# Kernel optimization log

Hardware: AMD Instinct MI355X
Metric: run time of the kernel (lower is better)

The kernel has to match this reference:

```python
import jax, jax.numpy as jnp
import numpy as np
from jax import lax

B, C, D, NH, H, W = 32, 768, 512, 4, 24, 24
HD = C // NH          # 192
FHW = H * W           # 576 (must equal 24*24 per o_proj_img2)


def _p(key, shape, scale=0.02):
    return scale * jax.random.normal(key, shape, dtype=jnp.float32)


def setup_inputs() -> dict:
    ks = jax.random.split(jax.random.key(0), 10)
    return dict(
        img_feats=jax.random.normal(ks[0], (B, C, H, W), jnp.float32),
        txt_feats=jax.random.normal(ks[1], (B, D), jnp.float32),
        fn_w=jnp.ones((C,), jnp.float32), fn_b=jnp.zeros((C,), jnp.float32),
        gn_w=jnp.ones((D,), jnp.float32), gn_b=jnp.zeros((D,), jnp.float32),
        qkv_img_w=_p(ks[2], (3 * C, C)),
        qkv_txt_w=_p(ks[3], (3 * C, D)),
        o_img_w=_p(ks[4], (C, C)), o_img_b=jnp.zeros((C,), jnp.float32),
        o_img2_w=_p(ks[5], (FHW, HD)), o_img2_b=jnp.zeros((FHW,), jnp.float32),
        ffn_norm_w=jnp.ones((C,), jnp.float32), ffn_norm_b=jnp.zeros((C,), jnp.float32),
        fc1_w=_p(ks[6], (C, C)),
        dw_w=_p(ks[7], (C, 1, 3, 3)),
        fc2_w=_p(ks[8], (C, C)),
    )


def layernorm2d(x, w, b, eps=1e-6):
    # normalize over channel dim (dim 1) of NCHW
    u = x.mean(1, keepdims=True)
    s = ((x - u) ** 2).mean(1, keepdims=True)
    x = (x - u) * lax.rsqrt(s + eps)
    return w[:, None, None] * x + b[:, None, None]


def l2norm_last(x, eps=1e-12):
    # F.normalize(x, dim=-1): divide by L2 norm clamped at eps
    n = jnp.sqrt(jnp.sum(x * x, axis=-1, keepdims=True))
    return x / jnp.maximum(n, eps)


def _forward(img_feats, txt_feats, fn_w, fn_b, gn_w, gn_b, qkv_img_w, qkv_txt_w,
             o_img_w, o_img_b, o_img2_w, o_img2_b, ffn_norm_w, ffn_norm_b,
             fc1_w, dw_w, fc2_w):
    x = layernorm2d(img_feats, fn_w, fn_b)
    # guide LayerNorm (torch default eps=1e-5, biased var)
    mu = txt_feats.mean(-1, keepdims=True)
    var = jnp.mean((txt_feats - mu) ** 2, axis=-1, keepdims=True)
    t = (txt_feats - mu) * lax.rsqrt(var + 1e-5) * gn_w + gn_b

    # qkv img: 1x1 conv; channel layout (ng nh hd) -> [B,3,NH,HD,F]
    qkv_img = jnp.einsum('bchw,oc->bohw', x, qkv_img_w).reshape(B, 3, NH, HD, FHW)
    q_img, k_img, v_img = qkv_img[:, 0], qkv_img[:, 1], qkv_img[:, 2]

    # qkv txt: layout 'b (nh (ng hd))' per the two rearranges -> [B,NH,3,HD]
    qkv_txt = (t @ qkv_txt_w.T).reshape(B, NH, 3, HD)
    q_txt, k_txt = qkv_txt[:, :, 0], qkv_txt[:, :, 1]

    # normalize over size-1 trailing dim == x / max(|x|, eps)  (sign-like)
    nq_txt = q_txt / jnp.maximum(jnp.abs(q_txt), 1e-12)          # [B,NH,HD]
    nk_img = l2norm_last(k_img)                                  # [B,NH,HD,F]
    # einsum('bnhd,bnhf->bnhf') with d of size 1 == broadcast multiply over h
    attn1 = jax.nn.softmax(nq_txt[..., None] * nk_img, axis=-1)  # [B,NH,HD,F]
    txt_on_img = jnp.einsum('bnhf,bngf->bnhg', attn1, v_img)     # [B,NH,HD,HD]

    nk_txt = k_txt / jnp.maximum(jnp.abs(k_txt), 1e-12)
    nq_img = l2norm_last(q_img)
    attn2 = jax.nn.softmax(nk_txt[..., None] * nq_img, axis=-1)
    txt_to_img2 = jnp.einsum('bnhf,bngf->bnhg', attn2, v_img)

    img = (txt_on_img + txt_to_img2).reshape(B, NH * HD, HD)     # [B,768,192]
    y = (img @ o_img2_w.T + o_img2_b).reshape(B, C, H, W)        # [B,768,24,24]
    out = jnp.einsum('bchw,oc->bohw', y, o_img_w) + o_img_b[None, :, None, None] + img_feats

    # ConvMlp FFN (mlp_times=1, bias=False convs, exact GELU)
    z = layernorm2d(out, ffn_norm_w, ffn_norm_b)
    z = jnp.einsum('bchw,oc->bohw', z, fc1_w)
    z = lax.conv_general_dilated(z, dw_w, (1, 1), 'SAME',
                                 feature_group_count=C,
                                 dimension_numbers=('NCHW', 'OIHW', 'NCHW'))
    z = jax.nn.gelu(z, approximate=False)
    z = jnp.einsum('bchw,oc->bohw', z, fc2_w)
    return out + z


def reference(img_feats, txt_feats, fn_w, fn_b, gn_w, gn_b, qkv_img_w, qkv_txt_w,
              o_img_w, o_img_b, o_img2_w, o_img2_b, ffn_norm_w, ffn_norm_b,
              fc1_w, dw_w, fc2_w):
    return _forward(img_feats, txt_feats, fn_w, fn_b, gn_w, gn_b, qkv_img_w,
                    qkv_txt_w, o_img_w, o_img_b, o_img2_w, o_img2_b,
                    ffn_norm_w, ffn_norm_b, fc1_w, dw_w, fc2_w)
```

## Files before the change

kernel.cpp:

```cpp
#include <hip/hip_runtime.h>

typedef unsigned short u16;
typedef __attribute__((ext_vector_type(8))) short short8_t;
typedef __attribute__((ext_vector_type(4))) float f32x4;
typedef __attribute__((ext_vector_type(4))) unsigned short u16x4;

static constexpr int cB   = 32;
static constexpr int cC   = 768;
static constexpr int cD   = 512;
static constexpr int cNH  = 4;
static constexpr int cHD  = 192;
static constexpr int cFHW = 576;
static constexpr int cC3  = 2304;

__device__ inline float us2f(u16 s) {
    union { unsigned int u; float f; } v; v.u = ((unsigned int)s) << 16; return v.f;
}
__device__ inline u16 f2bf(float f) {
    union { float f; unsigned int u; } v; v.f = f;
    unsigned int r = v.u + 0x7FFFu + ((v.u >> 16) & 1u);
    return (u16)(r >> 16);
}
__device__ inline float ldflex(const void* p, size_t i, int isf32) {
    return isf32 ? ((const float*)p)[i] : us2f(((const u16*)p)[i]);
}

__device__ inline void gload16(const void* g, void* l) {
    __builtin_amdgcn_global_load_lds(
        (const __attribute__((address_space(1))) void*)g,
        (__attribute__((address_space(3))) void*)l, 16, 0, 0);
}

__global__ void detect_kernel(const u16* __restrict__ raw, int* __restrict__ flags) {
    flags[0] = (raw[0] == 0x3F80u) ? 0 : 1;
}

struct FlatDesc { const void* src[12]; float* dst[12]; int off[13]; };
__global__ __launch_bounds__(256) void flatten_kernel(FlatDesc d, const int* __restrict__ flags) {
    const int isf = flags[0];
    const int gid = blockIdx.x * 256 + threadIdx.x;
    if (gid >= d.off[12]) return;
    int s = 0;
    #pragma unroll
    for (int i = 1; i < 12; i++) s += (gid >= d.off[i]) ? 1 : 0;
    const int j = gid - d.off[s];
    d.dst[s][j] = ldflex(d.src[s], j, isf);
}

__global__ __launch_bounds__(256) void cast_bf16_kernel(
    const void* __restrict__ src, u16* __restrict__ dst, int n, const int* __restrict__ flags)
{
    const int isf = flags[0];
    for (int i = blockIdx.x * 256 + threadIdx.x; i < n; i += gridDim.x * 256)
        dst[i] = isf ? f2bf(((const float*)src)[i]) : ((const u16*)src)[i];
}

__global__ __launch_bounds__(256) void fold_cast_kernel(
    const void* __restrict__ src, const float* __restrict__ gamma,
    u16* __restrict__ dst, int n, const int* __restrict__ flags)
{
    const int isf = flags[0];
    for (int i = blockIdx.x * 256 + threadIdx.x; i < n; i += gridDim.x * 256) {
        const int c = i % cC;
        dst[i] = f2bf(ldflex(src, i, isf) * gamma[c]);
    }
}

__global__ __launch_bounds__(64) void bias_fold_kernel(
    const void* __restrict__ W, const float* __restrict__ gamma, const float* __restrict__ beta,
    float* __restrict__ B1, float* __restrict__ B2, const int* __restrict__ flags)
{
    const int m = blockIdx.x, lane = threadIdx.x, isf = flags[0];
    float s1 = 0.f, s2 = 0.f;
    for (int c = lane; c < cC; c += 64) {
        const float wv = ldflex(W, (size_t)m * cC + c, isf);
        s1 += wv * beta[c]; s2 += wv * gamma[c];
    }
    #pragma unroll
    for (int o = 1; o < 64; o <<= 1) { s1 += __shfl_xor(s1, o, 64); s2 += __shfl_xor(s2, o, 64); }
    if (lane == 0) { B1[m] = s1; B2[m] = s2; }
}

__global__ __launch_bounds__(256) void transpose_kernel(
    const void* __restrict__ src, float* __restrict__ dst,
    int Mdim, int Kdim, const int* __restrict__ flags)
{
    __shared__ float t[32][33];
    const int isf = flags[0];
    const int k0 = blockIdx.x * 32, m0 = blockIdx.y * 32;
    const int x = threadIdx.x & 31, y = threadIdx.x >> 5;
    #pragma unroll
    for (int i = 0; i < 4; i++) {
        const int m = y + i * 8;
        t[m][x] = ldflex(src, (size_t)(m0 + m) * Kdim + k0 + x, isf);
    }
    __syncthreads();
    #pragma unroll
    for (int i = 0; i < 4; i++) {
        const int r = y + i * 8;
        dst[(size_t)(k0 + r) * Mdim + m0 + x] = t[x][r];
    }
}

__global__ __launch_bounds__(256) void txt_ln_kernel(
    const float* __restrict__ txt, const float* __restrict__ gw, const float* __restrict__ gb,
    float* __restrict__ tln)
{
    __shared__ float red[8];
    const int b = blockIdx.x, tid = threadIdx.x;
    const float v0 = txt[(size_t)b * cD + tid];
    const float v1 = txt[(size_t)b * cD + 256 + tid];
    float s = v0 + v1, ss = v0 * v0 + v1 * v1;
    #pragma unroll
    for (int o = 1; o < 64; o <<= 1) { s += __shfl_xor(s, o, 64); ss += __shfl_xor(ss, o, 64); }
    const int wid = tid >> 6, lane = tid & 63;
    if (lane == 0) { red[wid] = s; red[4 + wid] = ss; }
    __syncthreads();
    s  = red[0] + red[1] + red[2] + red[3];
    ss = red[4] + red[5] + red[6] + red[7];
    const float mean = s * (1.f / cD);
    const float var  = fmaxf(ss * (1.f / cD) - mean * mean, 0.f);
    const float r = rsqrtf(var + 1e-5f);
    tln[(size_t)b * cD + tid]       = (v0 - mean) * r * gw[tid]       + gb[tid];
    tln[(size_t)b * cD + 256 + tid] = (v1 - mean) * r * gw[tid + 256] + gb[tid + 256];
}

__global__ __launch_bounds__(256) void txt_gemm_kernel(
    const float* __restrict__ Wt, const float* __restrict__ tln, float* __restrict__ out)
{
    const int o  = blockIdx.x * 256 + threadIdx.x;
    const int b0 = blockIdx.y * 8;
    __shared__ float t[8][cD];
    for (int i = threadIdx.x; i < 8 * cD; i += 256)
        t[i >> 9][i & (cD - 1)] = tln[(size_t)(b0 + (i >> 9)) * cD + (i & (cD - 1))];
    __syncthreads();
    float acc[8] = {};
    #pragma unroll 2
    for (int k = 0; k < cD; k += 4) {
        const float w0 = Wt[(size_t)(k + 0) * cC3 + o];
        const float w1 = Wt[(size_t)(k + 1) * cC3 + o];
        const float w2 = Wt[(size_t)(k + 2) * cC3 + o];
        const float w3 = Wt[(size_t)(k + 3) * cC3 + o];
        #pragma unroll
        for (int b = 0; b < 8; b++) {
            const float4 tv = *(const float4*)&t[b][k];
            acc[b] += w0 * tv.x + w1 * tv.y + w2 * tv.z + w3 * tv.w;
        }
    }
    #pragma unroll
    for (int b = 0; b < 8; b++) out[(size_t)(b0 + b) * cC3 + o] = acc[b];
}

__global__ __launch_bounds__(1024) void ln_stats_kernel(
    const void* __restrict__ x, size_t xoff, float* __restrict__ mr,
    const int* __restrict__ flags)
{
    const int isf = flags[0];
    const int b = blockIdx.y;
    const int l = threadIdx.x & 63;
    const int f = (blockIdx.x << 6) + l;
    const int cg = threadIdx.x >> 6;
    const size_t base = xoff + (size_t)b * cC * cFHW + f;
    float s = 0.f, ss = 0.f;
    for (int c = cg; c < cC; c += 16) {
        float v = ldflex(x, base + (size_t)c * cFHW, isf);
        s += v; ss += v * v;
    }
    __shared__ float S[16][64], SS[16][64];
    S[cg][l] = s; SS[cg][l] = ss;
    __syncthreads();
    if (threadIdx.x < 64) {
        float su = 0.f, sq = 0.f;
        #pragma unroll
        for (int i = 0; i < 16; i++) { su += S[i][l]; sq += SS[i][l]; }
        const float mean = su * (1.f / cC);
        const float var  = fmaxf(sq * (1.f / cC) - mean * mean, 0.f);
        float* o = mr + ((size_t)b * cFHW + f) * 2;
        o[0] = mean; o[1] = rsqrtf(var + 1e-6f);
    }
}

__global__ __launch_bounds__(256) void ln_stats_rows_kernel(
    const u16* __restrict__ Xt, float* __restrict__ mr)
{
    const int wid = threadIdx.x >> 6, lane = threadIdx.x & 63;
    const size_t row = (size_t)blockIdx.x * 4 + wid;
    const u16* r = Xt + row * cC;
    float s = 0.f, ss = 0.f;
    const short8_t a = *(const short8_t*)(r + lane * 8);
    const u16x4 bq   = *(const u16x4*)(r + 512 + lane * 4);
    #pragma unroll
    for (int j = 0; j < 8; j++) { const float v = us2f((u16)a[j]); s += v; ss += v * v; }
    #pragma unroll
    for (int j = 0; j < 4; j++) { const float v = us2f(bq[j]); s += v; ss += v * v; }
    #pragma unroll
    for (int o = 1; o < 64; o <<= 1) { s += __shfl_xor(s, o, 64); ss += __shfl_xor(ss, o, 64); }
    if (lane == 0) {
        const float mean = s * (1.f / cC);
        const float var  = fmaxf(ss * (1.f / cC) - mean * mean, 0.f);
        mr[row * 2] = mean; mr[row * 2 + 1] = rsqrtf(var + 1e-6f);
    }
}

template <int XSRC>
__global__ __launch_bounds__(256) void prep_xt_kernel(
    const void* __restrict__ X, size_t xoff, u16* __restrict__ Xt,
    const float* __restrict__ mr, const float* __restrict__ lnw, const float* __restrict__ lnb,
    const int* __restrict__ flags)
{
    __shared__ float t[64][33];
    const int isf = (XSRC == 2) ? flags[0] : 1;
    const int f0 = blockIdx.x * 32, c0 = blockIdx.y * 64, b = blockIdx.z;
    const int tid = threadIdx.x;
    const int fx = tid & 31, cy = tid >> 5;
    const size_t base = (size_t)b * cC * cFHW;
    #pragma unroll
    for (int i = 0; i < 8; i++) {
        const int c = c0 + cy + i * 8;
        const size_t ei = base + (size_t)c * cFHW + f0 + fx;
        t[cy + i * 8][fx] = (XSRC == 2) ? ldflex(X, xoff + ei, isf) : ((const float*)X)[ei];
    }
    __syncthreads();
    const int cx = tid & 31, fy = tid >> 5;
    #pragma unroll
    for (int i = 0; i < 4; i++) {
        const int fl = fy + i * 8;
        const int f = f0 + fl;
        float v0 = t[cx * 2][fl], v1 = t[cx * 2 + 1][fl];
        if (XSRC == 2) {
            const float* mp = mr + ((size_t)b * cFHW + f) * 2;
            const float mean = mp[0], rst = mp[1];
            v0 = (v0 - mean) * rst * lnw[c0 + cx * 2]     + lnb[c0 + cx * 2];
            v1 = (v1 - mean) * rst * lnw[c0 + cx * 2 + 1] + lnb[c0 + cx * 2 + 1];
        }
        const unsigned int pk = (unsigned int)f2bf(v0) | ((unsigned int)f2bf(v1) << 16);
        *(unsigned int*)(Xt + base + (size_t)f * cC + c0 + cx * 2) = pk;
    }
}

template <int EPI>
__global__ __launch_bounds__(256, 2) void conv_mfma(
    const u16* __restrict__ Wb, const u16* __restrict__ Xt,
    float* __restrict__ outp, const float* __restrict__ bias_m,
    const void* __restrict__ resRaw, size_t resOff, const float* __restrict__ resF,
    u16* __restrict__ vout,
    const float* __restrict__ aff_mr, const float* __restrict__ aff_B1, const float* __restrict__ aff_B2,
    int M, int K, int Mt, const int* __restrict__ flags)
{
    const int nwg = 9 * Mt;
    int wg = blockIdx.x;
    {
        const int q = nwg >> 3, r = nwg & 7, x = wg & 7, idx = wg >> 3;
        wg = (x < r ? x * (q + 1) : r * (q + 1) + (x - r) * q) + idx;
    }
    const int xt = wg / Mt, yt = wg - xt * Mt;
    const int n0 = xt * 64, m0 = yt * 256, b = blockIdx.z;

    __shared__ __align__(16) u16 A_s[2][256 * 64];
    __shared__ __align__(16) u16 B_s[2][64 * 64];

    const int tid = threadIdx.x;
    const int w = tid >> 6, lane = tid & 63, lq = lane >> 4, lr = lane & 15;
    const int l8 = lane >> 3, c8 = lane & 7;
    const int xch = ((c8 ^ l8) << 4);

    const u16* wbase = Wb + (size_t)m0 * K;
    const u16* xbase = Xt + ((size_t)b * cFHW + n0) * K;

    f32x4 acc[4][4];
    #pragma unroll
    for (int i = 0; i < 4; i++)
        #pragma unroll
        for (int j = 0; j < 4; j++)
            acc[i][j] = (f32x4)0.f;

    const int nt = K >> 6;

    #pragma unroll
    for (int j = 0; j < 8; ++j) {
        const int r = w * 64 + j * 8 + l8;
        gload16((const char*)(wbase + (size_t)r * K) + xch, (char*)&A_s[0][(w * 64 + j * 8) * 64]);
    }
    #pragma unroll
    for (int j = 0; j < 2; ++j) {
        const int r = w * 16 + j * 8 + l8;
        gload16((const char*)(xbase + (size_t)r * K) + xch, (char*)&B_s[0][(w * 16 + j * 8) * 64]);
    }

    int buf = 0;
    #pragma unroll 1
    for (int t = 0; t < nt; ++t) {
        if (t + 1 < nt) {
            const int k0 = (t + 1) << 6;
            #pragma unroll
            for (int j = 0; j < 8; ++j) {
                const int r = w * 64 + j * 8 + l8;
                gload16((const char*)(wbase + (size_t)r * K + k0) + xch,
                        (char*)&A_s[buf ^ 1][(w * 64 + j * 8) * 64]);
            }
            #pragma unroll
            for (int j = 0; j < 2; ++j) {
                const int r = w * 16 + j * 8 + l8;
                gload16((const char*)(xbase + (size_t)r * K + k0) + xch,
                        (char*)&B_s[buf ^ 1][(w * 16 + j * 8) * 64]);
            }
            asm volatile("s_waitcnt vmcnt(10)" ::: "memory");
        } else {
            asm volatile("s_waitcnt vmcnt(0)" ::: "memory");
        }
        __builtin_amdgcn_s_barrier();
        __builtin_amdgcn_sched_barrier(0);
        __builtin_amdgcn_s_setprio(1);
        const u16* As = &A_s[buf][0];
        const u16* Bs = &B_s[buf][0];
        #pragma unroll
        for (int kk = 0; kk < 2; kk++) {
            short8_t af[4], bfr[4];
            #pragma unroll
            for (int fm = 0; fm < 4; fm++) {
                const int ml = w * 64 + fm * 16 + lr;
                af[fm] = *(const short8_t*)((const char*)As + ml * 128 + ((kk * 64 + lq * 16) ^ ((lr & 7) << 4)));
            }
            #pragma unroll
            for (int fn = 0; fn < 4; fn++) {
                const int nl = fn * 16 + lr;
                bfr[fn] = *(const short8_t*)((const char*)Bs + nl * 128 + ((kk * 64 + lq * 16) ^ ((lr & 7) << 4)));
            }
            #pragma unroll
            for (int fm = 0; fm < 4; fm++)
                #pragma unroll
                for (int fn = 0; fn < 4; fn++)
                    acc[fm][fn] = __builtin_amdgcn_mfma_f32_16x16x32_bf16(af[fm], bfr[fn], acc[fm][fn], 0, 0, 0);
        }
        __builtin_amdgcn_s_setprio(0);
        __builtin_amdgcn_s_barrier();
        buf ^= 1;
    }

    const int mrow0 = m0 + w * 64;

    if constexpr (EPI == 5) {
        #pragma unroll
        for (int fm = 0; fm < 4; fm++)
            #pragma unroll
            for (int fn = 0; fn < 4; fn++)
                #pragma unroll
                for (int i = 0; i < 4; i++) {
                    const int mg = mrow0 + fm * 16 + lq * 4 + i;
                    vout[((size_t)b * M + mg) * cFHW + n0 + fn * 16 + lr] = f2bf(acc[fm][fn][i]);
                }
        return;
    }
    if constexpr (EPI == 4) {
        float b1r[4][4], b2r[4][4];
        #pragma unroll
        for (int fm = 0; fm < 4; fm++)
            #pragma unroll
            for (int i = 0; i < 4; i++) {
                const int mg = mrow0 + fm * 16 + lq * 4 + i;
                b1r[fm][i] = aff_B1[mg];
                b2r[fm][i] = aff_B2[mg];
            }
        #pragma unroll
        for (int fn = 0; fn < 4; fn++) {
            const int nn = n0 + fn * 16 + lr;
            const float2 ms = *(const float2*)(aff_mr + ((size_t)b * cFHW + nn) * 2);
            const float sf = ms.y, mean_sf = ms.x * ms.y;
            #pragma unroll
            for (int fm = 0; fm < 4; fm++)
                #pragma unroll
                for (int i = 0; i < 4; i++) {
                    const int mg = mrow0 + fm * 16 + lq * 4 + i;
                    outp[((size_t)b * M + mg) * cFHW + nn] =
                        sf * acc[fm][fn][i] + b1r[fm][i] - mean_sf * b2r[fm][i];
                }
        }
        return;
    }
    if constexpr (EPI == 1) {
        const int isf = flags[0];
        #pragma unroll
        for (int fm = 0; fm < 4; fm++) {
            #pragma unroll
            for (int fn = 0; fn < 4; fn++) {
                const int nn = n0 + fn * 16 + lr;
                u16x4 pk;
                #pragma unroll
                for (int i = 0; i < 4; i++) {
                    const int mg = mrow0 + fm * 16 + lq * 4 + i;
                    const size_t o = ((size_t)b * M + mg) * cFHW + nn;
                    const float vv = acc[fm][fn][i] + bias_m[mg] + ldflex(resRaw, resOff + o, isf);
                    outp[o] = vv;
                    pk[i] = f2bf(vv);
                }
                *(u16x4*)(vout + ((size_t)b * cFHW + nn) * cC + (mrow0 + fm * 16 + lq * 4)) = pk;
            }
        }
        return;
    }
    #pragma unroll
    for (int fm = 0; fm < 4; fm++) {
        #pragma unroll
        for (int fn = 0; fn < 4; fn++) {
            #pragma unroll
            for (int i = 0; i < 4; i++) {
                const int mg = mrow0 + fm * 16 + lq * 4 + i;
                const size_t o = ((size_t)b * M + mg) * cFHW + n0 + fn * 16 + lr;
                float vv = acc[fm][fn][i];
                if constexpr (EPI == 2) vv += resF[o];
                outp[o] = vv;
            }
        }
    }
}

__global__ __launch_bounds__(64) void attn_p_kernel(
    const u16* __restrict__ qkv, const float* __restrict__ tq, u16* __restrict__ Pbf)
{
    const int idx = blockIdx.x;
    const int h = idx % cHD;
    const int bn = idx / cHD;
    const int n = bn & 3, b = bn >> 2;
    const int lane = threadIdx.x;
    const u16* qrow = qkv + ((size_t)b * cC3 + n * cHD + h) * cFHW;
    const u16* krow = qkv + ((size_t)b * cC3 + cC + n * cHD + h) * cFHW;
    float kvr[9], qvr[9];
    #pragma unroll
    for (int j = 0; j < 9; j++) {
        kvr[j] = us2f(krow[lane + j * 64]);
        qvr[j] = us2f(qrow[lane + j * 64]);
    }
    float ssk = 0.f, mink = 3.0e38f, maxk = -3.0e38f;
    float ssq = 0.f, minq = 3.0e38f, maxq = -3.0e38f;
    #pragma unroll
    for (int j = 0; j < 9; j++) {
        const float kv = kvr[j]; ssk += kv * kv; maxk = fmaxf(maxk, kv); mink = fminf(mink, kv);
        const float qv = qvr[j]; ssq += qv * qv; maxq = fmaxf(maxq, qv); minq = fminf(minq, qv);
    }
    #pragma unroll
    for (int o = 1; o < 64; o <<= 1) {
        ssk += __shfl_xor(ssk, o, 64); ssq += __shfl_xor(ssq, o, 64);
        maxk = fmaxf(maxk, __shfl_xor(maxk, o, 64)); mink = fminf(mink, __shfl_xor(mink, o, 64));
        maxq = fmaxf(maxq, __shfl_xor(maxq, o, 64)); minq = fminf(minq, __shfl_xor(minq, o, 64));
    }
    const float qt = tq[(size_t)b * cC3 + n * 3 * cHD + h];
    const float kt = tq[(size_t)b * cC3 + n * 3 * cHD + cHD + h];
    const float sign1 = qt / fmaxf(fabsf(qt), 1e-12f);
    const float sign2 = kt / fmaxf(fabsf(kt), 1e-12f);
    const float a1 = sign1 / fmaxf(sqrtf(ssk), 1e-12f);
    const float a2 = sign2 / fmaxf(sqrtf(ssq), 1e-12f);
    const float m1 = fmaxf(a1 * maxk, a1 * mink);
    const float m2 = fmaxf(a2 * maxq, a2 * minq);
    float e1[9], e2[9];
    float z1 = 0.f, z2 = 0.f;
    #pragma unroll
    for (int j = 0; j < 9; j++) {
        e1[j] = expf(a1 * kvr[j] - m1); z1 += e1[j];
        e2[j] = expf(a2 * qvr[j] - m2); z2 += e2[j];
    }
    #pragma unroll
    for (int o = 1; o < 64; o <<= 1) { z1 += __shfl_xor(z1, o, 64); z2 += __shfl_xor(z2, o, 64); }
    const float iz1 = 1.f / z1, iz2 = 1.f / z2;
    u16* prow = Pbf + ((size_t)b * cC + n * cHD + h) * cFHW;
    #pragma unroll
    for (int j = 0; j < 9; j++)
        prow[lane + j * 64] = f2bf(e1[j] * iz1 + e2[j] * iz2);
}

__global__ __launch_bounds__(256, 2) void pv_mfma(
    const u16* __restrict__ P, const u16* __restrict__ qkv, u16* __restrict__ img, int nbn)
{
    const int nwg = 3 * nbn;
    int wg = blockIdx.x;
    {
        const int q = nwg >> 3, r = nwg & 7, x = wg & 7, idx = wg >> 3;
        wg = (x < r ? x * (q + 1) : r * (q + 1) + (x - r) * q) + idx;
    }
    const int bn = wg / 3, gt = wg - bn * 3;
    const int g0 = gt * 64;
    const int b = bn >> 2, n = bn & 3;

    __shared__ __align__(16) u16 A_s[2][192 * 64];
    __shared__ __align__(16) u16 B_s[2][64 * 64];

    const int tid = threadIdx.x;
    const int w = tid >> 6, lane = tid & 63, lq = lane >> 4, lr = lane & 15;
    const int l8 = lane >> 3, c8 = lane & 7;
    const int xch = ((c8 ^ l8) << 4);

    const u16* pbase = P + ((size_t)b * cC + n * cHD) * cFHW;
    const u16* vbase = qkv + ((size_t)b * cC3 + 2 * cC + n * cHD + g0) * cFHW;

    f32x4 acc[3][4];
    #pragma unroll
    for (int i = 0; i < 3; i++)
        #pragma unroll
        for (int j = 0; j < 4; j++)
            acc[i][j] = (f32x4)0.f;

    const int nt = cFHW / 64;

    #pragma unroll
    for (int j = 0; j < 6; ++j) {
        const int r = w * 48 + j * 8 + l8;
        gload16((const char*)(pbase + (size_t)r * cFHW) + xch, (char*)&A_s[0][(w * 48 + j * 8) * 64]);
    }
    #pragma unroll
    for (int j = 0; j < 2; ++j) {
        const int r = w * 16 + j * 8 + l8;
        gload16((const char*)(vbase + (size_t)r * cFHW) + xch, (char*)&B_s[0][(w * 16 + j * 8) * 64]);
    }

    int buf = 0;
    #pragma unroll 1
    for (int t = 0; t < nt; ++t) {
        if (t + 1 < nt) {
            const int k0 = (t + 1) << 6;
            #pragma unroll
            for (int j = 0; j < 6; ++j) {
                const int r = w * 48 + j * 8 + l8;
                gload16((const char*)(pbase + (size_t)r * cFHW + k0) + xch,
                        (char*)&A_s[buf ^ 1][(w * 48 + j * 8) * 64]);
            }
            #pragma unroll
            for (int j = 0; j < 2; ++j) {
                const int r = w * 16 + j * 8 + l8;
                gload16((const char*)(vbase + (size_t)r * cFHW + k0) + xch,
                        (char*)&B_s[buf ^ 1][(w * 16 + j * 8) * 64]);
            }
            asm volatile("s_waitcnt vmcnt(8)" ::: "memory");
        } else {
            asm volatile("s_waitcnt vmcnt(0)" ::: "memory");
        }
        __builtin_amdgcn_s_barrier();
        __builtin_amdgcn_sched_barrier(0);
        __builtin_amdgcn_s_setprio(1);
        const u16* As = &A_s[buf][0];
        const u16* Bs = &B_s[buf][0];
        #pragma unroll
        for (int kk = 0; kk < 2; kk++) {
            short8_t af[3], bfr[4];
            #pragma unroll
            for (int fm = 0; fm < 3; fm++) {
                const int ml = w * 48 + fm * 16 + lr;
                af[fm] = *(const short8_t*)((const char*)As + ml * 128 + ((kk * 64 + lq * 16) ^ ((lr & 7) << 4)));
            }
            #pragma unroll
            for (int fn = 0; fn < 4; fn++) {
                const int nl = fn * 16 + lr;
                bfr[fn] = *(const short8_t*)((const char*)Bs + nl * 128 + ((kk * 64 + lq * 16) ^ ((lr & 7) << 4)));
            }
            #pragma unroll
            for (int fm = 0; fm < 3; fm++)
                #pragma unroll
                for (int fn = 0; fn < 4; fn++)
                    acc[fm][fn] = __builtin_amdgcn_mfma_f32_16x16x32_bf16(af[fm], bfr[fn], acc[fm][fn], 0, 0, 0);
        }
        __builtin_amdgcn_s_setprio(0);
        __builtin_amdgcn_s_barrier();
        buf ^= 1;
    }

    #pragma unroll
    for (int fm = 0; fm < 3; fm++)
        #pragma unroll
        for (int fn = 0; fn < 4; fn++)
            #pragma unroll
            for (int i = 0; i < 4; i++) {
                const int mm = w * 48 + fm * 16 + lq * 4 + i;
                img[((size_t)b * cC + n * cHD + mm) * cHD + g0 + fn * 16 + lr] = f2bf(acc[fm][fn][i]);
            }
}

__global__ __launch_bounds__(256, 2) void y_mfma(
    const u16* __restrict__ img, const u16* __restrict__ o2w,
    const float* __restrict__ bias_n, u16* __restrict__ Xt)
{
    const int nwg = 9 * 3;
    int wg = blockIdx.x;
    {
        const int q = nwg >> 3, r = nwg & 7, x = wg & 7, idx = wg >> 3;
        wg = (x < r ? x * (q + 1) : r * (q + 1) + (x - r) * q) + idx;
    }
    const int xt = wg / 3, yt = wg - xt * 3;
    const int n0 = xt * 64, m0 = yt * 256, b = blockIdx.z;
    constexpr int K = cHD;

    __shared__ __align__(16) u16 A_s[2][256 * 64];
    __shared__ __align__(16) u16 B_s[2][64 * 64];

    const int tid = threadIdx.x;
    const int w = tid >> 6, lane = tid & 63, lq = lane >> 4, lr = lane & 15;
    const int l8 = lane >> 3, c8 = lane & 7;
    const int xch = ((c8 ^ l8) << 4);

    const u16* abase = img + ((size_t)b * cC + m0) * K;
    const u16* bbase = o2w + (size_t)n0 * K;

    f32x4 acc[4][4];
    #pragma unroll
    for (int i = 0; i < 4; i++)
        #pragma unroll
        for (int j = 0; j < 4; j++)
            acc[i][j] = (f32x4)0.f;

    const int nt = K >> 6;

    #pragma unroll
    for (int j = 0; j < 8; ++j) {
        const int r = w * 64 + j * 8 + l8;
        gload16((const char*)(abase + (size_t)r * K) + xch, (char*)&A_s[0][(w * 64 + j * 8) * 64]);
    }
    #pragma unroll
    for (int j = 0; j < 2; ++j) {
        const int r = w * 16 + j * 8 + l8;
        gload16((const char*)(bbase + (size_t)r * K) + xch, (char*)&B_s[0][(w * 16 + j * 8) * 64]);
    }

    int buf = 0;
    #pragma unroll 1
    for (int t = 0; t < nt; ++t) {
        if (t + 1 < nt) {
            const int k0 = (t + 1) << 6;
            #pragma unroll
            for (int j = 0; j < 8; ++j) {
                const int r = w * 64 + j * 8 + l8;
                gload16((const char*)(abase + (size_t)r * K + k0) + xch,
                        (char*)&A_s[buf ^ 1][(w * 64 + j * 8) * 64]);
            }
            #pragma unroll
            for (int j = 0; j < 2; ++j) {
                const int r = w * 16 + j * 8 + l8;
                gload16((const char*)(bbase + (size_t)r * K + k0) + xch,
                        (char*)&B_s[buf ^ 1][(w * 16 + j * 8) * 64]);
            }
            asm volatile("s_waitcnt vmcnt(10)" ::: "memory");
        } else {
            asm volatile("s_waitcnt vmcnt(0)" ::: "memory");
        }
        __builtin_amdgcn_s_barrier();
        __builtin_amdgcn_sched_barrier(0);
        __builtin_amdgcn_s_setprio(1);
        const u16* As = &A_s[buf][0];
        const u16* Bs = &B_s[buf][0];
        #pragma unroll
        for (int kk = 0; kk < 2; kk++) {
            short8_t af[4], bfr[4];
            #pragma unroll
            for (int fm = 0; fm < 4; fm++) {
                const int ml = w * 64 + fm * 16 + lr;
                af[fm] = *(const short8_t*)((const char*)As + ml * 128 + ((kk * 64 + lq * 16) ^ ((lr & 7) << 4)));
            }
            #pragma unroll
            for (int fn = 0; fn < 4; fn++) {
                const int nl = fn * 16 + lr;
                bfr[fn] = *(const short8_t*)((const char*)Bs + nl * 128 + ((kk * 64 + lq * 16) ^ ((lr & 7) << 4)));
            }
            #pragma unroll
            for (int fm = 0; fm < 4; fm++)
                #pragma unroll
                for (int fn = 0; fn < 4; fn++)
                    acc[fm][fn] = __builtin_amdgcn_mfma_f32_16x16x32_bf16(af[fm], bfr[fn], acc[fm][fn], 0, 0, 0);
        }
        __builtin_amdgcn_s_setprio(0);
        __builtin_amdgcn_s_barrier();
        buf ^= 1;
    }

    #pragma unroll
    for (int fm = 0; fm < 4; fm++) {
        #pragma unroll
        for (int fn = 0; fn < 4; fn++) {
            const int nn = n0 + fn * 16 + lr;
            const float bn_ = bias_n[nn];
            u16x4 pk;
            #pragma unroll
            for (int i = 0; i < 4; i++) pk[i] = f2bf(acc[fm][fn][i] + bn_);
            const int mm = m0 + w * 64 + fm * 16 + lq * 4;
            *(u16x4*)(Xt + ((size_t)b * cFHW + nn) * cC + mm) = pk;
        }
    }
}

__global__ __launch_bounds__(576) void dwconv_gelu_kernel(
    const float* __restrict__ X, const float* __restrict__ w, float* __restrict__ Y)
{
    const int c = blockIdx.x, b = blockIdx.y;
    __shared__ float t[26][28];
    const int tid = threadIdx.x;
    float* tf = &t[0][0];
    for (int i = tid; i < 26 * 28; i += 576) tf[i] = 0.f;
    __syncthreads();
    const size_t base = ((size_t)b * cC + c) * cFHW;
    const int x = tid % 24, y = tid / 24;
    t[y + 1][x + 1] = X[base + tid];
    __syncthreads();
    float w9[9];
    #pragma unroll
    for (int j = 0; j < 9; j++) w9[j] = w[c * 9 + j];
    float s = 0.f;
    #pragma unroll
    for (int dy = 0; dy < 3; dy++)
        #pragma unroll
        for (int dx = 0; dx < 3; dx++)
            s += w9[dy * 3 + dx] * t[y + dy][x + dx];
    const float g = 0.5f * s * (1.f + erff(s * 0.70710678118654752f));
    Y[base + tid] = g;
}

extern "C" void kernel_launch(void* const* d_in, const int* in_sizes, int n_in,
                              void* d_out, int out_size, void* d_ws, size_t ws_size,
                              hipStream_t stream)
{
    char* p = (char*)d_ws;
    auto allocB = [&](size_t bytes) { char* r = p; p += (bytes + 255) & ~(size_t)255; return r; };
    float* c_txt   = (float*)allocB((size_t)cB * cD * 4);
    float* c_fnw   = (float*)allocB(cC * 4);
    float* c_fnb   = (float*)allocB(cC * 4);
    float* c_gnw   = (float*)allocB(cD * 4);
    float* c_gnb   = (float*)allocB(cD * 4);
    float* c_oib   = (float*)allocB(cC * 4);
    float* c_oi2w  = (float*)allocB((size_t)cFHW * cHD * 4);
    float* c_oi2b  = (float*)allocB(cFHW * 4);
    float* c_ffnw  = (float*)allocB(cC * 4);
    float* c_ffnb  = (float*)allocB(cC * 4);
    float* c_dw    = (float*)allocB(cC * 9 * 4);
    u16*   w_qkv_bf = (u16*)allocB((size_t)cC3 * cC * 2);
    u16*   w_oi_bf  = (u16*)allocB((size_t)cC * cC * 2);
    u16*   w_fc1_bf = (u16*)allocB((size_t)cC * cC * 2);
    u16*   w_fc2_bf = (u16*)allocB((size_t)cC * cC * 2);
    u16*   w_o2w_bf = (u16*)allocB((size_t)cFHW * cHD * 2);
    float* t_qkvtw = (float*)allocB((size_t)cD * cC3 * 4);
    float* tln     = (float*)allocB((size_t)cB * cD * 4);
    int*   flags   = (int*)allocB(256);
    float* tq      = (float*)allocB((size_t)cB * cC3 * 4);
    float* mr1     = (float*)allocB((size_t)cB * cFHW * 2 * 4);
    float* mr2     = (float*)allocB((size_t)cB * cFHW * 2 * 4);
    float* b1f     = (float*)allocB(cC * 4);
    float* b2f     = (float*)allocB(cC * 4);
    const size_t fixedBytes = (size_t)(p - (char*)d_ws);
    auto needBytes = [&](int Q) {
        return fixedBytes
             + (size_t)Q * (cC3 + cC) * cFHW * 2ull
             + (size_t)Q * cC * cFHW * 4ull * 2ull
             + (size_t)Q * cC * cHD * 2ull
             + (size_t)Q * cC * cFHW * 2ull
             + 8192;
    };
    int Q = 8;
    if (ws_size >= needBytes(32)) Q = 32;
    else if (ws_size >= needBytes(16)) Q = 16;
    const size_t QCF = (size_t)Q * cC * cFHW;
    char*  qkvreg = allocB((size_t)Q * (cC3 + cC) * cFHW * 2);
    u16*   qkvbf = (u16*)qkvreg;
    u16*   Pbf   = (u16*)(qkvreg + (size_t)Q * cC3 * cFHW * 2);
    float* A2    = (float*)qkvreg;
    float* A0    = (float*)allocB(QCF * 4);
    float* A1    = (float*)allocB(QCF * 4);
    u16*   imgbf = (u16*)allocB((size_t)Q * cC * cHD * 2);
    u16*   XtA   = (u16*)allocB(QCF * 2);
    (void)in_sizes; (void)n_in; (void)out_size;

    detect_kernel<<<1, 1, 0, stream>>>((const u16*)d_in[2], flags);

    FlatDesc fd;
    const void* srcs[11] = { d_in[1], d_in[2], d_in[3], d_in[4], d_in[5],
                             d_in[9], d_in[10], d_in[11], d_in[12], d_in[13], d_in[15] };
    float* dsts[11]      = { c_txt, c_fnw, c_fnb, c_gnw, c_gnb,
                             c_oib, c_oi2w, c_oi2b, c_ffnw, c_ffnb, c_dw };
    const int ns[11]     = { cB * cD, cC, cC, cD, cD,
                             cC, cFHW * cHD, cFHW, cC, cC, cC * 9 };
    int tot = 0;
    for (int i = 0; i < 11; i++) { fd.src[i] = srcs[i]; fd.dst[i] = dsts[i]; fd.off[i] = tot; tot += ns[i]; }
    fd.src[11] = srcs[0]; fd.dst[11] = dsts[0];
    fd.off[11] = tot; fd.off[12] = tot;
    flatten_kernel<<<(tot + 255) / 256, 256, 0, stream>>>(fd, flags);

    cast_bf16_kernel<<<512, 256, 0, stream>>>(d_in[6],  w_qkv_bf, cC3 * cC, flags);
    cast_bf16_kernel<<<256, 256, 0, stream>>>(d_in[8],  w_oi_bf,  cC * cC, flags);
    fold_cast_kernel<<<256, 256, 0, stream>>>(d_in[14], c_ffnw, w_fc1_bf, cC * cC, flags);
    cast_bf16_kernel<<<256, 256, 0, stream>>>(d_in[16], w_fc2_bf, cC * cC, flags);
    cast_bf16_kernel<<<128, 256, 0, stream>>>(d_in[10], w_o2w_bf, cFHW * cHD, flags);
    bias_fold_kernel<<<cC, 64, 0, stream>>>(d_in[14], c_ffnw, c_ffnb, b1f, b2f, flags);

    transpose_kernel<<<dim3(cD / 32, cC3 / 32), 256, 0, stream>>>(d_in[7], t_qkvtw, cC3, cD, flags);
    txt_ln_kernel<<<cB, 256, 0, stream>>>(c_txt, c_gnw, c_gnb, tln);
    txt_gemm_kernel<<<dim3(cC3 / 256, cB / 8), 256, 0, stream>>>(t_qkvtw, tln, tq);

    for (int q0 = 0; q0 < cB; q0 += Q) {
        const size_t off = (size_t)q0 * cC * cFHW;
        u16* XtB = (u16*)((float*)d_out + off);
        ln_stats_kernel<<<dim3(9, Q), 1024, 0, stream>>>(d_in[0], off, mr1, flags);
        prep_xt_kernel<2><<<dim3(cFHW / 32, cC / 64, Q), 256, 0, stream>>>(
            d_in[0], off, XtA, mr1, c_fnw, c_fnb, flags);
        conv_mfma<5><<<dim3(9 * (cC3 / 256), 1, Q), 256, 0, stream>>>(
            w_qkv_bf, XtA, nullptr, nullptr, nullptr, 0, nullptr, qkvbf,
            nullptr, nullptr, nullptr, cC3, cC, cC3 / 256, flags);
        attn_p_kernel<<<Q * cNH * cHD, 64, 0, stream>>>(qkvbf, tq + (size_t)q0 * cC3, Pbf);
        pv_mfma<<<3 * Q * cNH, 256, 0, stream>>>(Pbf, qkvbf, imgbf, Q * cNH);
        y_mfma<<<dim3(27, 1, Q), 256, 0, stream>>>(imgbf, w_o2w_bf, c_oi2b, XtA);
        conv_mfma<1><<<dim3(9 * (cC / 256), 1, Q), 256, 0, stream>>>(
            w_oi_bf, XtA, A0, c_oib, d_in[0], off, nullptr, XtB,
            nullptr, nullptr, nullptr, cC, cC, cC / 256, flags);
        ln_stats_rows_kernel<<<Q * cFHW / 4, 256, 0, stream>>>(XtB, mr2);
        conv_mfma<4><<<dim3(9 * (cC / 256), 1, Q), 256, 0, stream>>>(
            w_fc1_bf, XtB, A2, nullptr, nullptr, 0, nullptr, nullptr,
            mr2, b1f, b2f, cC, cC, cC / 256, flags);
        dwconv_gelu_kernel<<<dim3(cC, Q), 576, 0, stream>>>(A2, c_dw, A1);
        prep_xt_kernel<0><<<dim3(cFHW / 32, cC / 64, Q), 256, 0, stream>>>(
            A1, 0, XtA, nullptr, nullptr, nullptr, flags);
        conv_mfma<2><<<dim3(9 * (cC / 256), 1, Q), 256, 0, stream>>>(
            w_fc2_bf, XtA, (float*)d_out + off, nullptr, nullptr, 0, A0, nullptr,
            nullptr, nullptr, nullptr, cC, cC, cC / 256, flags);
    }
}
```

Measured before the change: 705.0 us.

## Fuse LN stats with transpose prep and store FFN intermediates in bf16

Merges the input LayerNorm statistics kernel and the normalize-transpose kernel into one kernel, so each block computes stats for 16 spatial positions and then writes the normalized bf16 transposed rows. The fc1 output and the depthwise-conv/GELU output are now stored as bf16 instead of fp32, which halves the intermediate traffic through dwconv and the final transpose. The cost is extra rounding of the FFN intermediates, and the fused prep's second pass does strided column reads with 2-byte scalar writes, which may coalesce poorly.

```diff
diff --git a/kernel.cpp b/kernel.cpp
--- a/kernel.cpp
+++ b/kernel.cpp
@@ -151,32 +151,50 @@
     for (int b = 0; b < 8; b++) out[(size_t)(b0 + b) * cC3 + o] = acc[b];
 }
 
-__global__ __launch_bounds__(1024) void ln_stats_kernel(
-    const void* __restrict__ x, size_t xoff, float* __restrict__ mr,
+__global__ __launch_bounds__(256) void ln_prep_kernel(
+    const void* __restrict__ X, size_t xoff, u16* __restrict__ Xt,
+    const float* __restrict__ lnw, const float* __restrict__ lnb,
     const int* __restrict__ flags)
 {
     const int isf = flags[0];
-    const int b = blockIdx.y;
-    const int l = threadIdx.x & 63;
-    const int f = (blockIdx.x << 6) + l;
-    const int cg = threadIdx.x >> 6;
-    const size_t base = xoff + (size_t)b * cC * cFHW + f;
-    float s = 0.f, ss = 0.f;
-    for (int c = cg; c < cC; c += 16) {
-        float v = ldflex(x, base + (size_t)c * cFHW, isf);
-        s += v; ss += v * v;
-    }
-    __shared__ float S[16][64], SS[16][64];
-    S[cg][l] = s; SS[cg][l] = ss;
+    const int f0 = blockIdx.x * 16, b = blockIdx.y;
+    const int tid = threadIdx.x;
+    const size_t base  = xoff + (size_t)b * cC * cFHW;
+    const size_t obase = (size_t)b * cC * cFHW;
+    __shared__ float S[16][17], SS[16][17];
+    __shared__ float MR[16][2];
+    {
+        const int fx = tid & 15, cg = tid >> 4;
+        float s = 0.f, ss = 0.f;
+        for (int c = cg; c < cC; c += 16) {
+            const float v = ldflex(X, base + (size_t)c * cFHW + f0 + fx, isf);
+            s += v; ss += v * v;
+        }
+        S[cg][fx] = s; SS[cg][fx] = ss;
+    }
     __syncthreads();
-    if (threadIdx.x < 64) {
+    if (tid < 16) {
         float su = 0.f, sq = 0.f;
         #pragma unroll
-        for (int i = 0; i < 16; i++) { su += S[i][l]; sq += SS[i][l]; }
+        for (int i = 0; i < 16; i++) { su += S[i][tid]; sq += SS[i][tid]; }
         const float mean = su * (1.f / cC);
         const float var  = fmaxf(sq * (1.f / cC) - mean * mean, 0.f);
-        float* o = mr + ((size_t)b * cFHW + f) * 2;
-        o[0] = mean; o[1] = rsqrtf(var + 1e-6f);
+        MR[tid][0] = mean; MR[tid][1] = rsqrtf(var + 1e-6f);
+    }
+    __syncthreads();
+    const int cx = tid & 63, fy = tid >> 6;
+    #pragma unroll
+    for (int ff = 0; ff < 4; ff++) {
+        const int fl = fy * 4 + ff;
+        const float mean = MR[fl][0], rst = MR[fl][1];
+        u16* orow = Xt + obase + (size_t)(f0 + fl) * cC;
+        const size_t rrow = base + (size_t)(f0 + fl);
+        #pragma unroll
+        for (int j = 0; j < 12; j++) {
+            const int c = cx + j * 64;
+            const float v = ldflex(X, rrow + (size_t)c * cFHW, isf);
+            orow[c] = f2bf((v - mean) * rst * lnw[c] + lnb[c]);
+        }
     }
 }
 
@@ -204,12 +222,9 @@
 
 template <int XSRC>
 __global__ __launch_bounds__(256) void prep_xt_kernel(
-    const void* __restrict__ X, size_t xoff, u16* __restrict__ Xt,
-    const float* __restrict__ mr, const float* __restrict__ lnw, const float* __restrict__ lnb,
-    const int* __restrict__ flags)
+    const void* __restrict__ X, u16* __restrict__ Xt)
 {
     __shared__ float t[64][33];
-    const int isf = (XSRC == 2) ? flags[0] : 1;
     const int f0 = blockIdx.x * 32, c0 = blockIdx.y * 64, b = blockIdx.z;
     const int tid = threadIdx.x;
     const int fx = tid & 31, cy = tid >> 5;
@@ -218,7 +233,7 @@
     for (int i = 0; i < 8; i++) {
         const int c = c0 + cy + i * 8;
         const size_t ei = base + (size_t)c * cFHW + f0 + fx;
-        t[cy + i * 8][fx] = (XSRC == 2) ? ldflex(X, xoff + ei, isf) : ((const float*)X)[ei];
+        t[cy + i * 8][fx] = (XSRC == 3) ? us2f(((const u16*)X)[ei]) : ((const float*)X)[ei];
     }
     __syncthreads();
     const int cx = tid & 31, fy = tid >> 5;
@@ -226,13 +241,7 @@
     for (int i = 0; i < 4; i++) {
         const int fl = fy + i * 8;
         const int f = f0 + fl;
-        float v0 = t[cx * 2][fl], v1 = t[cx * 2 + 1][fl];
-        if (XSRC == 2) {
-            const float* mp = mr + ((size_t)b * cFHW + f) * 2;
-            const float mean = mp[0], rst = mp[1];
-            v0 = (v0 - mean) * rst * lnw[c0 + cx * 2]     + lnb[c0 + cx * 2];
-            v1 = (v1 - mean) * rst * lnw[c0 + cx * 2 + 1] + lnb[c0 + cx * 2 + 1];
-        }
+        const float v0 = t[cx * 2][fl], v1 = t[cx * 2 + 1][fl];
         const unsigned int pk = (unsigned int)f2bf(v0) | ((unsigned int)f2bf(v1) << 16);
         *(unsigned int*)(Xt + base + (size_t)f * cC + c0 + cx * 2) = pk;
     }
@@ -371,8 +380,8 @@
                 #pragma unroll
                 for (int i = 0; i < 4; i++) {
                     const int mg = mrow0 + fm * 16 + lq * 4 + i;
-                    outp[((size_t)b * M + mg) * cFHW + nn] =
-                        sf * acc[fm][fn][i] + b1r[fm][i] - mean_sf * b2r[fm][i];
+                    vout[((size_t)b * M + mg) * cFHW + nn] =
+                        f2bf(sf * acc[fm][fn][i] + b1r[fm][i] - mean_sf * b2r[fm][i]);
                 }
         }
         return;
@@ -683,7 +692,7 @@
 }
 
 __global__ __launch_bounds__(576) void dwconv_gelu_kernel(
-    const float* __restrict__ X, const float* __restrict__ w, float* __restrict__ Y)
+    const u16* __restrict__ X, const float* __restrict__ w, u16* __restrict__ Y)
 {
     const int c = blockIdx.x, b = blockIdx.y;
     __shared__ float t[26][28];
@@ -693,7 +702,7 @@
     __syncthreads();
     const size_t base = ((size_t)b * cC + c) * cFHW;
     const int x = tid % 24, y = tid / 24;
-    t[y + 1][x + 1] = X[base + tid];
+    t[y + 1][x + 1] = us2f(X[base + tid]);
     __syncthreads();
     float w9[9];
     #pragma unroll
@@ -705,7 +714,7 @@
         for (int dx = 0; dx < 3; dx++)
             s += w9[dy * 3 + dx] * t[y + dy][x + dx];
     const float g = 0.5f * s * (1.f + erff(s * 0.70710678118654752f));
-    Y[base + tid] = g;
+    Y[base + tid] = f2bf(g);
 }
 
 extern "C" void kernel_launch(void* const* d_in, const int* in_sizes, int n_in,
@@ -734,7 +743,6 @@
     float* tln     = (float*)allocB((size_t)cB * cD * 4);
     int*   flags   = (int*)allocB(256);
     float* tq      = (float*)allocB((size_t)cB * cC3 * 4);
-    float* mr1     = (float*)allocB((size_t)cB * cFHW * 2 * 4);
     float* mr2     = (float*)allocB((size_t)cB * cFHW * 2 * 4);
     float* b1f     = (float*)allocB(cC * 4);
     float* b2f     = (float*)allocB(cC * 4);
@@ -742,7 +750,8 @@
     auto needBytes = [&](int Q) {
         return fixedBytes
              + (size_t)Q * (cC3 + cC) * cFHW * 2ull
-             + (size_t)Q * cC * cFHW * 4ull * 2ull
+             + (size_t)Q * cC * cFHW * 4ull
+             + (size_t)Q * cC * cFHW * 2ull
              + (size_t)Q * cC * cHD * 2ull
              + (size_t)Q * cC * cFHW * 2ull
              + 8192;
@@ -754,9 +763,9 @@
     char*  qkvreg = allocB((size_t)Q * (cC3 + cC) * cFHW * 2);
     u16*   qkvbf = (u16*)qkvreg;
     u16*   Pbf   = (u16*)(qkvreg + (size_t)Q * cC3 * cFHW * 2);
-    float* A2    = (float*)qkvreg;
+    u16*   A2bf  = (u16*)qkvreg;
     float* A0    = (float*)allocB(QCF * 4);
-    float* A1    = (float*)allocB(QCF * 4);
+    u16*   A1bf  = (u16*)allocB(QCF * 2);
     u16*   imgbf = (u16*)allocB((size_t)Q * cC * cHD * 2);
     u16*   XtA   = (u16*)allocB(QCF * 2);
     (void)in_sizes; (void)n_in; (void)out_size;
@@ -790,9 +799,8 @@
     for (int q0 = 0; q0 < cB; q0 += Q) {
         const size_t off = (size_t)q0 * cC * cFHW;
         u16* XtB = (u16*)((float*)d_out + off);
-        ln_stats_kernel<<<dim3(9, Q), 1024, 0, stream>>>(d_in[0], off, mr1, flags);
-        prep_xt_kernel<2><<<dim3(cFHW / 32, cC / 64, Q), 256, 0, stream>>>(
-            d_in[0], off, XtA, mr1, c_fnw, c_fnb, flags);
+        ln_prep_kernel<<<dim3(cFHW / 16, Q), 256, 0, stream>>>(
+            d_in[0], off, XtA, c_fnw, c_fnb, flags);
         conv_mfma<5><<<dim3(9 * (cC3 / 256), 1, Q), 256, 0, stream>>>(
             w_qkv_bf, XtA, nullptr, nullptr, nullptr, 0, nullptr, qkvbf,
             nullptr, nullptr, nullptr, cC3, cC, cC3 / 256, flags);
@@ -804,11 +812,10 @@
             nullptr, nullptr, nullptr, cC, cC, cC / 256, flags);
         ln_stats_rows_kernel<<<Q * cFHW / 4, 256, 0, stream>>>(XtB, mr2);
         conv_mfma<4><<<dim3(9 * (cC / 256), 1, Q), 256, 0, stream>>>(
-            w_fc1_bf, XtB, A2, nullptr, nullptr, 0, nullptr, nullptr,
+            w_fc1_bf, XtB, nullptr, nullptr, nullptr, 0, nullptr, A2bf,
             mr2, b1f, b2f, cC, cC, cC / 256, flags);
-        dwconv_gelu_kernel<<<dim3(cC, Q), 576, 0, stream>>>(A2, c_dw, A1);
-        prep_xt_kernel<0><<<dim3(cFHW / 32, cC / 64, Q), 256, 0, stream>>>(
-            A1, 0, XtA, nullptr, nullptr, nullptr, flags);
+        dwconv_gelu_kernel<<<dim3(cC, Q), 576, 0, stream>>>(A2bf, c_dw, A1bf);
+        prep_xt_kernel<3><<<dim3(cFHW / 32, cC / 64, Q), 256, 0, stream>>>(A1bf, XtA);
         conv_mfma<2><<<dim3(9 * (cC / 256), 1, Q), 256, 0, stream>>>(
             w_fc2_bf, XtA, (float*)d_out + off, nullptr, nullptr, 0, A0, nullptr,
             nullptr, nullptr, nullptr, cC, cC, cC / 256, flags);
```

Measured after the change: 720.3 us. +2.2%, slower.
